# Kernel optimization log

Hardware: AMD Instinct MI355X
Metric: run time of the kernel (lower is better)

Reference implementation:

```python
import jax, jax.numpy as jnp
import numpy as np

N = 50000   # nodes
E = 800000  # edges before self-loops
H = 4       # heads
D = 64      # num_h_feats (per-head out dim of hidden layers)
C = 2       # num_classes
NEG = 0.2   # DGL GATConv leaky_relu negative_slope
EPS = 1e-5  # BatchNorm eps


def setup_inputs() -> dict:
    key = jax.random.key(0)
    ks = jax.random.split(key, 16)
    inp = {}
    inp['feats'] = jax.random.normal(ks[0], (N, 9), jnp.float32)
    inp['W1'] = jax.random.normal(ks[1], (9, H * D), jnp.float32) * 0.1
    inp['al1'] = jax.random.normal(ks[2], (H, D), jnp.float32) * 0.1
    inp['ar1'] = jax.random.normal(ks[3], (H, D), jnp.float32) * 0.1
    inp['b1'] = jnp.zeros((H, D), jnp.float32)
    inp['Wm'] = jax.random.normal(ks[4], (D, H * D), jnp.float32) * 0.1
    inp['alm'] = jax.random.normal(ks[5], (H, D), jnp.float32) * 0.1
    inp['arm'] = jax.random.normal(ks[6], (H, D), jnp.float32) * 0.1
    inp['bm'] = jnp.zeros((H, D), jnp.float32)
    inp['W2'] = jax.random.normal(ks[7], (D, H * C), jnp.float32) * 0.1
    inp['al2'] = jax.random.normal(ks[8], (H, C), jnp.float32) * 0.1
    inp['ar2'] = jax.random.normal(ks[9], (H, C), jnp.float32) * 0.1
    inp['b2'] = jnp.zeros((H, C), jnp.float32)
    inp['gamma'] = jnp.ones((D,), jnp.float32)
    inp['beta'] = jnp.zeros((D,), jnp.float32)
    inp['src'] = jax.random.randint(ks[10], (E,), 0, N, jnp.int32)
    inp['dst'] = jax.random.randint(ks[11], (E,), 0, N, jnp.int32)
    return inp


def gat_layer(x, W, al, ar, b, src, dst, out_d):
    """DGL GATConv: linear -> per-edge attention -> dst-softmax -> scatter-sum."""
    n = x.shape[0]
    z = (x @ W).reshape(n, H, out_d)                 # [N, H, Dout]
    el = jnp.sum(z * al, axis=-1)                    # [N, H] attn on src
    er = jnp.sum(z * ar, axis=-1)                    # [N, H] attn on dst
    e = jax.nn.leaky_relu(el[src] + er[dst], NEG)    # [E, H]
    m = jax.ops.segment_max(e, dst, num_segments=n)  # per-dst max (stable softmax)
    a = jnp.exp(e - m[dst])
    s = jax.ops.segment_sum(a, dst, num_segments=n)
    alpha = a / s[dst]                               # [E, H]
    out = jax.ops.segment_sum(alpha[:, :, None] * z[src], dst, num_segments=n)
    return out + b                                   # [N, H, Dout]


def batchnorm(h, gamma, beta):
    mu = jnp.mean(h, axis=0)
    var = jnp.var(h, axis=0)
    return (h - mu) * jax.lax.rsqrt(var + EPS) * gamma + beta


def reference(feats, W1, al1, ar1, b1, Wm, alm, arm, bm, W2, al2, ar2, b2,
              gamma, beta, src, dst):
    # dgl.add_self_loop
    loop = jnp.arange(N, dtype=src.dtype)
    s = jnp.concatenate([src, loop])
    d = jnp.concatenate([dst, loop])
    h = gat_layer(feats, W1, al1, ar1, b1, s, d, D).sum(axis=1)  # head-sum
    h = batchnorm(h, gamma, beta)
    h = gat_layer(h, Wm, alm, arm, bm, s, d, D).sum(axis=1)
    h = batchnorm(h, gamma, beta)
    o = gat_layer(h, W2, al2, ar2, b2, s, d, C).sum(axis=1)      # [N, C]
    return o
```

## Files before the change

### kernel.cpp

```cpp
#include <hip/hip_runtime.h>
#include <hip/hip_bf16.h>

typedef __hip_bfloat16 bf16;
typedef __bf16 bf16x8 __attribute__((ext_vector_type(8)));
typedef float f32x4 __attribute__((ext_vector_type(4)));
typedef _Float16 h16;
typedef _Float16 h16x4 __attribute__((ext_vector_type(4)));

#define LOG2E 1.44269504088896340736f

__device__ __forceinline__ float b2f(bf16 v) { return __bfloat162float(v); }

__device__ __forceinline__ float ldin(const void* p, size_t i, int isb) {
    return isb ? b2f(((const bf16*)p)[i]) : ((const float*)p)[i];
}
__device__ __forceinline__ unsigned short f2bfbits(float f) {
    bf16 v = __float2bfloat16(f);
    return *(unsigned short*)&v;
}

__global__ __launch_bounds__(256) void fused_prep_lin1_kernel(
    const void* __restrict__ feats, const void* __restrict__ W1,
    const void* __restrict__ Wm,
    const void* __restrict__ al1, const void* __restrict__ ar1,
    const void* __restrict__ alm, const void* __restrict__ arm,
    const unsigned* __restrict__ gbits,
    const int* __restrict__ dstv, int* __restrict__ deg,
    unsigned short* __restrict__ WmT,
    float* __restrict__ alfm, float* __restrict__ arfm,
    h16* __restrict__ zh, float* __restrict__ zc,
    float* __restrict__ el, float* __restrict__ er,
    int* __restrict__ flag, int Nn, int E, int NT) {
    __shared__ h16 zs[16 * 256];
    int isb = (gbits[0] == 0x3F803F80u) ? 1 : 0;
    int tid = threadIdx.x;
    long t = (long)blockIdx.x * 256 + tid;
    if (t == 0) *flag = isb;

    long b1 = (long)E + 2048;
    long b2 = b1 + 256;
    long b3 = b2 + 268;
    if (t < E) {
        atomicAdd(&deg[dstv[t]], 1);
    } else if (t < b1) {
        long u = t - E;
        int col = (int)(u >> 3), k0 = ((int)u & 7) * 8;
        union { unsigned short us[8]; uint4 v; } o;
#pragma unroll
        for (int j = 0; j < 8; j++) {
            int k = k0 + j;
            o.us[j] = f2bfbits(ldin(Wm, (size_t)k * 256 + col, isb));
        }
        *(uint4*)(WmT + u * 8) = o.v;
    } else if (t < b2) {
        int u = (int)(t - b1);
        alfm[u] = ldin(alm, u, isb) * LOG2E;
        arfm[u] = ldin(arm, u, isb) * LOG2E;
    } else if (t < b3) {
        long u = t - b2;
        if (u < 4) {
            el[(size_t)Nn * 4 + u] = -1e30f;
        } else if (u < 260) {
            ((unsigned short*)zh)[(size_t)Nn * 256 + (u - 4)] = 0;
        } else {
            zc[(size_t)Nn * 8 + (u - 260)] = 0.f;
        }
    }

    if (blockIdx.x >= NT) return;
    int w = tid >> 6;
    int l = tid & 63;
    int quad = l >> 4, lc = l & 15;
    int node0 = blockIdx.x * 16;

    int mrow = node0 + lc; if (mrow >= Nn) mrow = Nn - 1;
    union { unsigned short s[8]; bf16x8 v; } ua;
#pragma unroll
    for (int j = 0; j < 8; j++) {
        int k = quad * 8 + j;
        ua.s[j] = (k < 9) ? f2bfbits(ldin(feats, (size_t)mrow * 9 + k, isb))
                          : (unsigned short)0;
    }
    bf16x8 a0 = ua.v;

    float pe[4] = {0.f, 0.f, 0.f, 0.f}, pr[4] = {0.f, 0.f, 0.f, 0.f};
    int row0 = quad * 4;
#pragma unroll
    for (int ct = 0; ct < 4; ++ct) {
        int col = w * 64 + ct * 16 + lc;
        union { unsigned short s[8]; bf16x8 v; } ub;
#pragma unroll
        for (int j = 0; j < 8; j++) {
            int k = quad * 8 + j;
            ub.s[j] = (k < 9) ? f2bfbits(ldin(W1, (size_t)k * 256 + col, isb))
                              : (unsigned short)0;
        }
        f32x4 c = {0.f, 0.f, 0.f, 0.f};
        c = __builtin_amdgcn_mfma_f32_16x16x32_bf16(a0, ub.v, c, 0, 0, 0);
        float av = ldin(al1, col, isb) * LOG2E;
        float rv = ldin(ar1, col, isb) * LOG2E;
#pragma unroll
        for (int r = 0; r < 4; ++r) {
            pe[r] = fmaf(c[r], av, pe[r]);
            pr[r] = fmaf(c[r], rv, pr[r]);
            zs[(row0 + r) * 256 + col] = (h16)c[r];
        }
    }
#pragma unroll
    for (int o = 1; o < 16; o <<= 1) {
#pragma unroll
        for (int r = 0; r < 4; ++r) {
            pe[r] += __shfl_xor(pe[r], o);
            pr[r] += __shfl_xor(pr[r], o);
        }
    }
    if (lc == 0) {
#pragma unroll
        for (int r = 0; r < 4; ++r) {
            int n = node0 + row0 + r;
            if (n < Nn) { el[n * 4 + w] = pe[r]; er[n * 4 + w] = pr[r]; }
        }
    }
    __syncthreads();
#pragma unroll
    for (int it = 0; it < 2; ++it) {
        int flat = it * 2048 + tid * 8;
        int row = flat >> 8;
        if (node0 + row < Nn)
            *(uint4*)(zh + (size_t)node0 * 256 + flat) = *(const uint4*)(zs + flat);
    }
}

__global__ __launch_bounds__(256) void scan1_kernel(
    const int* __restrict__ deg, int* __restrict__ off, int* __restrict__ bsum, int Nn) {
    __shared__ int s[256];
    int t = threadIdx.x, i = blockIdx.x * 256 + t;
    int v = (i < Nn) ? ((deg[i] + 3) & ~3) : 0;
    s[t] = v; __syncthreads();
#pragma unroll
    for (int o = 1; o < 256; o <<= 1) {
        int a = (t >= o) ? s[t - o] : 0;
        __syncthreads();
        s[t] += a;
        __syncthreads();
    }
    if (i < Nn) off[i] = s[t];
    if (t == 255) bsum[blockIdx.x] = s[255];
}

__global__ __launch_bounds__(256) void scan3_kernel(
    const int* __restrict__ deg, int* __restrict__ off, int* __restrict__ cur,
    int* __restrict__ adj, const int* __restrict__ bsum, int Nn, int NB) {
    __shared__ int s[256];
    int t = threadIdx.x;
    int v = (t < NB) ? bsum[t] : 0;
    s[t] = v; __syncthreads();
#pragma unroll
    for (int o = 1; o < 256; o <<= 1) {
        int a = (t >= o) ? s[t - o] : 0;
        __syncthreads();
        s[t] += a;
        __syncthreads();
    }
    s[t] -= v;
    __syncthreads();
    int base = s[blockIdx.x];
    int i = blockIdx.x * 256 + t;
    if (i < Nn) {
        int d = deg[i], pd = (d + 3) & ~3;
        int ex = off[i] - pd + base;
        off[i] = ex;
        cur[i] = ex;
        for (int j = d; j < pd; j++) adj[ex + j] = Nn;
        if (i == Nn - 1) {
            int tot = ex + pd;
            off[Nn] = tot;
            for (int j = 0; j < 32; j++) adj[tot + j] = Nn;
        }
    }
}

__global__ __launch_bounds__(256) void scatter_kernel(
    const int* __restrict__ src, const int* __restrict__ dst,
    int* __restrict__ cur, int* __restrict__ adj, int E) {
    int t = blockIdx.x * 256 + threadIdx.x;
    if (t < E) {
        int p = atomicAdd(&cur[dst[t]], 1);
        adj[p] = src[t];
    }
}

__global__ __launch_bounds__(256) void lin_mfma_bn_kernel(
    const float* __restrict__ x,
    const float* __restrict__ bnsum, const float* __restrict__ bnsumsq,
    const void* __restrict__ gamma, const void* __restrict__ beta,
    const unsigned short* __restrict__ WT,
    const float* __restrict__ alf, const float* __restrict__ arf,
    h16* __restrict__ zh, float* __restrict__ el, float* __restrict__ er,
    const int* __restrict__ flag, int Nn) {
    __shared__ h16 zs[16 * 256];
    __shared__ __align__(16) float scs[64], shs[64];
    int tid = threadIdx.x;
    if (tid < 64) {
        int isb = *flag;
        float inv_n = 1.f / (float)Nn;
        float mu = bnsum[tid] * inv_n;
        float var = bnsumsq[tid] * inv_n - mu * mu;
        float s = rsqrtf(var + 1e-5f) * ldin(gamma, tid, isb);
        scs[tid] = s;
        shs[tid] = ldin(beta, tid, isb) - mu * s;
    }
    __syncthreads();

    int w = tid >> 6;
    int l = tid & 63;
    int quad = l >> 4, lc = l & 15;
    int node0 = blockIdx.x * 16;

    int mrow = node0 + lc; if (mrow >= Nn) mrow = Nn - 1;
    const float* xr = x + (size_t)mrow * 64 + quad * 8;
    float4 f0 = ((const float4*)xr)[0];
    float4 f1 = ((const float4*)xr)[1];
    float4 f2 = ((const float4*)(xr + 32))[0];
    float4 f3 = ((const float4*)(xr + 32))[1];
    float4 s0 = ((const float4*)(scs + quad * 8))[0];
    float4 s1 = ((const float4*)(scs + quad * 8))[1];
    float4 s2 = ((const float4*)(scs + 32 + quad * 8))[0];
    float4 s3 = ((const float4*)(scs + 32 + quad * 8))[1];
    float4 h0 = ((const float4*)(shs + quad * 8))[0];
    float4 h1 = ((const float4*)(shs + quad * 8))[1];
    float4 h2 = ((const float4*)(shs + 32 + quad * 8))[0];
    float4 h3 = ((const float4*)(shs + 32 + quad * 8))[1];

    union { bf16x8 v; unsigned short s[8]; } ua, ub;
    ua.s[0] = f2bfbits(fmaf(f0.x, s0.x, h0.x));
    ua.s[1] = f2bfbits(fmaf(f0.y, s0.y, h0.y));
    ua.s[2] = f2bfbits(fmaf(f0.z, s0.z, h0.z));
    ua.s[3] = f2bfbits(fmaf(f0.w, s0.w, h0.w));
    ua.s[4] = f2bfbits(fmaf(f1.x, s1.x, h1.x));
    ua.s[5] = f2bfbits(fmaf(f1.y, s1.y, h1.y));
    ua.s[6] = f2bfbits(fmaf(f1.z, s1.z, h1.z));
    ua.s[7] = f2bfbits(fmaf(f1.w, s1.w, h1.w));
    ub.s[0] = f2bfbits(fmaf(f2.x, s2.x, h2.x));
    ub.s[1] = f2bfbits(fmaf(f2.y, s2.y, h2.y));
    ub.s[2] = f2bfbits(fmaf(f2.z, s2.z, h2.z));
    ub.s[3] = f2bfbits(fmaf(f2.w, s2.w, h2.w));
    ub.s[4] = f2bfbits(fmaf(f3.x, s3.x, h3.x));
    ub.s[5] = f2bfbits(fmaf(f3.y, s3.y, h3.y));
    ub.s[6] = f2bfbits(fmaf(f3.z, s3.z, h3.z));
    ub.s[7] = f2bfbits(fmaf(f3.w, s3.w, h3.w));
    bf16x8 a0 = ua.v, a1 = ub.v;

    float pe[4] = {0.f, 0.f, 0.f, 0.f}, pr[4] = {0.f, 0.f, 0.f, 0.f};
    int row0 = quad * 4;
#pragma unroll
    for (int ct = 0; ct < 4; ++ct) {
        int col = w * 64 + ct * 16 + lc;
        const bf16x8* wb = (const bf16x8*)(WT + (size_t)col * 64);
        bf16x8 b0 = wb[quad];
        bf16x8 b1 = wb[quad + 4];
        f32x4 c = {0.f, 0.f, 0.f, 0.f};
        c = __builtin_amdgcn_mfma_f32_16x16x32_bf16(a0, b0, c, 0, 0, 0);
        c = __builtin_amdgcn_mfma_f32_16x16x32_bf16(a1, b1, c, 0, 0, 0);
        float av = alf[col], rv = arf[col];
#pragma unroll
        for (int r = 0; r < 4; ++r) {
            pe[r] = fmaf(c[r], av, pe[r]);
            pr[r] = fmaf(c[r], rv, pr[r]);
            zs[(row0 + r) * 256 + col] = (h16)c[r];
        }
    }
#pragma unroll
    for (int o = 1; o < 16; o <<= 1) {
#pragma unroll
        for (int r = 0; r < 4; ++r) {
            pe[r] += __shfl_xor(pe[r], o);
            pr[r] += __shfl_xor(pr[r], o);
        }
    }
    if (lc == 0) {
#pragma unroll
        for (int r = 0; r < 4; ++r) {
            int n = node0 + row0 + r;
            if (n < Nn) { el[n * 4 + w] = pe[r]; er[n * 4 + w] = pr[r]; }
        }
    }
    __syncthreads();
#pragma unroll
    for (int it = 0; it < 2; ++it) {
        int flat = it * 2048 + threadIdx.x * 8;
        int row = flat >> 8;
        if (node0 + row < Nn)
            *(uint4*)(zh + (size_t)node0 * 256 + flat) = *(const uint4*)(zs + flat);
    }
}

__global__ __launch_bounds__(256) void bnstats_kernel(
    const float* __restrict__ x, float* __restrict__ bnsum, float* __restrict__ bnsumsq,
    int Nn) {
    __shared__ float ssum[4][64], ssq[4][64];
    int tid = threadIdx.x;
    int d = tid & 63, r = tid >> 6;
    float s = 0.f, q = 0.f;
    int stride = gridDim.x * 4;
    for (int n = blockIdx.x * 4 + r; n < Nn; n += stride) {
        float v = x[(size_t)n * 64 + d];
        s += v;
        q = fmaf(v, v, q);
    }
    ssum[r][d] = s; ssq[r][d] = q;
    __syncthreads();
    if (tid < 64) {
        float ts = ssum[0][tid] + ssum[1][tid] + ssum[2][tid] + ssum[3][tid];
        float tq = ssq[0][tid] + ssq[1][tid] + ssq[2][tid] + ssq[3][tid];
        atomicAdd(&bnsum[tid], ts);
        atomicAdd(&bnsumsq[tid], tq);
    }
}

__global__ __launch_bounds__(256) void lin3_kernel(
    const float* __restrict__ x,
    const float* __restrict__ bnsum, const float* __restrict__ bnsumsq,
    const void* __restrict__ gamma, const void* __restrict__ beta,
    const void* __restrict__ W, const void* __restrict__ al, const void* __restrict__ ar,
    float* __restrict__ zc, float* __restrict__ el, float* __restrict__ er,
    const int* __restrict__ flag, int Nn) {
    __shared__ __align__(16) float scs[64], shs[64];
    int isb = *flag;
    int tid = threadIdx.x;
    if (tid < 64) {
        float inv_n = 1.f / (float)Nn;
        float mu = bnsum[tid] * inv_n;
        float var = bnsumsq[tid] * inv_n - mu * mu;
        float s = rsqrtf(var + 1e-5f) * ldin(gamma, tid, isb);
        scs[tid] = s;
        shs[tid] = ldin(beta, tid, isb) - mu * s;
    }
    __syncthreads();
    int t = blockIdx.x * 256 + tid;
    if (t >= Nn * 4) return;
    int n = t >> 2, h = t & 3;
    const float4* xr4 = (const float4*)(x + (size_t)n * 64);
    float a0 = 0.f, a1 = 0.f;
#pragma unroll 4
    for (int kk = 0; kk < 16; kk++) {
        float4 xv = xr4[kk];
        int k = kk * 4;
        float xn;
        xn = fmaf(xv.x, scs[k + 0], shs[k + 0]);
        a0 += xn * ldin(W, (k + 0) * 8 + h * 2, isb);
        a1 += xn * ldin(W, (k + 0) * 8 + h * 2 + 1, isb);
        xn = fmaf(xv.y, scs[k + 1], shs[k + 1]);
        a0 += xn * ldin(W, (k + 1) * 8 + h * 2, isb);
        a1 += xn * ldin(W, (k + 1) * 8 + h * 2 + 1, isb);
        xn = fmaf(xv.z, scs[k + 2], shs[k + 2]);
        a0 += xn * ldin(W, (k + 2) * 8 + h * 2, isb);
        a1 += xn * ldin(W, (k + 2) * 8 + h * 2 + 1, isb);
        xn = fmaf(xv.w, scs[k + 3], shs[k + 3]);
        a0 += xn * ldin(W, (k + 3) * 8 + h * 2, isb);
        a1 += xn * ldin(W, (k + 3) * 8 + h * 2 + 1, isb);
    }
    zc[n * 8 + h * 2 + 0] = a0;
    zc[n * 8 + h * 2 + 1] = a1;
    el[t] = (a0 * ldin(al, h * 2, isb) + a1 * ldin(al, h * 2 + 1, isb)) * LOG2E;
    er[t] = (a0 * ldin(ar, h * 2, isb) + a1 * ldin(ar, h * 2 + 1, isb)) * LOG2E;
}

#define GATH(ev, zv, sv)                                        \
    {                                                           \
        ev[0] = el[sv.x * 4 + h]; ev[1] = el[sv.y * 4 + h];     \
        ev[2] = el[sv.z * 4 + h]; ev[3] = el[sv.w * 4 + h];     \
        zv[0] = zrow[(size_t)sv.x * 64 + l];                    \
        zv[1] = zrow[(size_t)sv.y * 64 + l];                    \
        zv[2] = zrow[(size_t)sv.z * 64 + l];                    \
        zv[3] = zrow[(size_t)sv.w * 64 + l];                    \
    }
#define COMP(ev, zv)                                        \
    {                                                       \
        _Pragma("unroll") for (int j = 0; j < 4; j++) {     \
            float e = ev[j] + ern;                          \
            e = fmaxf(e, 0.2f * e);                         \
            float wj = __builtin_amdgcn_exp2f(e);           \
            lsum += wj;                                     \
            acc.x = fmaf(wj, (float)zv[j].x, acc.x);        \
            acc.y = fmaf(wj, (float)zv[j].y, acc.y);        \
            acc.z = fmaf(wj, (float)zv[j].z, acc.z);        \
            acc.w = fmaf(wj, (float)zv[j].w, acc.w);        \
        }                                                   \
    }

__global__ __launch_bounds__(256) void gat_agg64_kernel(
    const h16* __restrict__ zh, const float* __restrict__ el, const float* __restrict__ er,
    const int* __restrict__ off, const int* __restrict__ adj, const void* __restrict__ bias,
    float* __restrict__ x, const int* __restrict__ flag, int Nn, int total_waves) {
    int isb = *flag;
    int tid = threadIdx.x;
    int l = tid & 63;
    int h = l >> 4;
    int gw = blockIdx.x * 4 + (tid >> 6);
    const h16x4* zrow = (const h16x4*)zh;

    float4 bsl;
    bsl.x = ldin(bias, l * 4 + 0, isb);
    bsl.y = ldin(bias, l * 4 + 1, isb);
    bsl.z = ldin(bias, l * 4 + 2, isb);
    bsl.w = ldin(bias, l * 4 + 3, isb);

    if (gw >= Nn) return;

    int n = gw;
    int fs0 = off[n], fs1 = off[n + 1];
    float fel = el[n * 4 + h], fer = er[n * 4 + h];
    int4 fsv = *(const int4*)(adj + fs0);

    while (true) {
        int s0 = fs0;
        int nb = (fs1 - fs0) >> 2;
        float eln = fel, ern = fer;
        int4 svA = fsv;
        h16x4 zself = zrow[(size_t)n * 64 + l];
        int nn = n + total_waves;
        if (nn < Nn) {
            fs0 = off[nn]; fs1 = off[nn + 1];
            fel = el[nn * 4 + h]; fer = er[nn * 4 + h];
            fsv = *(const int4*)(adj + fs0);
        }

        float e0 = eln + ern;
        e0 = fmaxf(e0, 0.2f * e0);
        float w0 = __builtin_amdgcn_exp2f(e0);
        float lsum = w0;
        float4 acc = {0.f, 0.f, 0.f, 0.f};

        if (nb > 0) {
            float evA[4], evB[4];
            h16x4 zvA[4], zvB[4];
            GATH(evA, zvA, svA);
            int4 svB = *(const int4*)(adj + s0 + 4);
            int k = 0;
            while (true) {
                if (k + 1 < nb) GATH(evB, zvB, svB);
                svA = *(const int4*)(adj + s0 + (k + 2) * 4);
                COMP(evA, zvA);
                if (++k >= nb) break;
                if (k + 1 < nb) GATH(evA, zvA, svA);
                svB = *(const int4*)(adj + s0 + (k + 2) * 4);
                COMP(evB, zvB);
                if (++k >= nb) break;
            }
        }

        acc.x = fmaf(w0, (float)zself.x, acc.x);
        acc.y = fmaf(w0, (float)zself.y, acc.y);
        acc.z = fmaf(w0, (float)zself.z, acc.z);
        acc.w = fmaf(w0, (float)zself.w, acc.w);

        float inv = 1.f / lsum;
        float4 r;
        r.x = fmaf(acc.x, inv, bsl.x);
        r.y = fmaf(acc.y, inv, bsl.y);
        r.z = fmaf(acc.z, inv, bsl.z);
        r.w = fmaf(acc.w, inv, bsl.w);
#pragma unroll
        for (int o = 16; o < 64; o <<= 1) {
            r.x += __shfl_xor(r.x, o);
            r.y += __shfl_xor(r.y, o);
            r.z += __shfl_xor(r.z, o);
            r.w += __shfl_xor(r.w, o);
        }
        if (h == 0) ((float4*)(x + (size_t)n * 64))[l & 15] = r;
        if (nn >= Nn) break;
        n = nn;
    }
}
#undef GATH
#undef COMP

#define GATH2(ev, zv, sv)                                       \
    {                                                           \
        ev[0] = el[sv.x * 4 + h]; zv[0] = zc2[sv.x * 4 + h];    \
        ev[1] = el[sv.y * 4 + h]; zv[1] = zc2[sv.y * 4 + h];    \
        ev[2] = el[sv.z * 4 + h]; zv[2] = zc2[sv.z * 4 + h];    \
        ev[3] = el[sv.w * 4 + h]; zv[3] = zc2[sv.w * 4 + h];    \
    }
#define COMP2(ev, zv)                                       \
    {                                                       \
        _Pragma("unroll") for (int j = 0; j < 4; j++) {     \
            float e = ev[j] + er_nh;                        \
            e = fmaxf(e, 0.2f * e);                         \
            float w = __builtin_amdgcn_exp2f(e);            \
            lsum += w;                                      \
            a0 = fmaf(w, zv[j].x, a0);                      \
            a1 = fmaf(w, zv[j].y, a1);                      \
        }                                                   \
    }

__global__ __launch_bounds__(256) void gat_agg2_kernel(
    const float* __restrict__ zc, const float* __restrict__ el, const float* __restrict__ er,
    const int* __restrict__ off, const int* __restrict__ adj, const void* __restrict__ bias,
    void* __restrict__ out, const int* __restrict__ flag, int Nn) {
    int isb = *flag;
    int t = blockIdx.x * 256 + threadIdx.x;
    if (t >= Nn * 4) return;
    int n = t >> 2, h = t & 3;
    const float2* zc2 = (const float2*)zc;
    float er_nh = er[n * 4 + h];
    float e0 = el[n * 4 + h] + er_nh;
    e0 = fmaxf(e0, 0.2f * e0);
    float w0 = __builtin_amdgcn_exp2f(e0);
    float lsum = w0;
    float2 zn = zc2[n * 4 + h];
    float a0 = w0 * zn.x, a1 = w0 * zn.y;
    int s0 = off[n];
    int nb = (off[n + 1] - s0) >> 2;
    if (nb > 0) {
        float evA[4], evB[4], evC[4];
        float2 zvA[4], zvB[4], zvC[4];
        int4 svA = *(const int4*)(adj + s0);
        GATH2(evA, zvA, svA);
        int4 svB = *(const int4*)(adj + s0 + 4);
        if (nb > 1) GATH2(evB, zvB, svB);
        int4 svC = *(const int4*)(adj + s0 + 8);
        int k = 0;
        while (true) {
            if (k + 2 < nb) GATH2(evC, zvC, svC);
            svA = *(const int4*)(adj + s0 + (k + 3) * 4);
            COMP2(evA, zvA);
            if (++k >= nb) break;
            if (k + 2 < nb) GATH2(evA, zvA, svA);
            svB = *(const int4*)(adj + s0 + (k + 3) * 4);
            COMP2(evB, zvB);
            if (++k >= nb) break;
            if (k + 2 < nb) GATH2(evB, zvB, svB);
            svC = *(const int4*)(adj + s0 + (k + 3) * 4);
            COMP2(evC, zvC);
            if (++k >= nb) break;
        }
    }
    float inv = 1.f / lsum;
    float v0 = fmaf(a0, inv, ldin(bias, h * 2 + 0, isb));
    float v1 = fmaf(a1, inv, ldin(bias, h * 2 + 1, isb));
#pragma unroll
    for (int o = 1; o < 4; o <<= 1) {
        v0 += __shfl_xor(v0, o);
        v1 += __shfl_xor(v1, o);
    }
    if (h == 0) {
        if (isb) {
            ((bf16*)out)[n * 2 + 0] = __float2bfloat16(v0);
            ((bf16*)out)[n * 2 + 1] = __float2bfloat16(v1);
        } else {
            ((float*)out)[n * 2 + 0] = v0;
            ((float*)out)[n * 2 + 1] = v1;
        }
    }
}
#undef GATH2
#undef COMP2

extern "C" void kernel_launch(void* const* d_in, const int* in_sizes, int n_in,
                              void* d_out, int out_size, void* d_ws, size_t ws_size,
                              hipStream_t stream) {
    const void* feats = d_in[0];
    const void* W1    = d_in[1];
    const void* al1   = d_in[2];
    const void* ar1   = d_in[3];
    const void* b1    = d_in[4];
    const void* Wm    = d_in[5];
    const void* alm   = d_in[6];
    const void* arm   = d_in[7];
    const void* bm    = d_in[8];
    const void* W2    = d_in[9];
    const void* al2   = d_in[10];
    const void* ar2   = d_in[11];
    const void* b2v   = d_in[12];
    const void* gamma = d_in[13];
    const void* beta  = d_in[14];
    const int*  src   = (const int*)d_in[15];
    const int*  dst   = (const int*)d_in[16];

    int Nn = in_sizes[0] / 9;
    int E  = in_sizes[15];

    float* ws = (float*)d_ws;
    h16*   zh   = (h16*)ws;
    float* zc   = ws + (size_t)(Nn + 1) * 128;
    float* el   = zc + (size_t)Nn * 8 + 8;
    float* er   = el + (size_t)Nn * 4 + 4;
    float* x    = er + (size_t)Nn * 4;
    int*   deg  = (int*)(x + (size_t)Nn * 64);
    float* bns1 = (float*)(deg + Nn);
    float* bnq1 = bns1 + 64;
    float* bns2 = bnq1 + 64;
    float* bnq2 = bns2 + 64;
    size_t msetBytes = (size_t)Nn * 4 + 256 * 4;
    float* alfm = bnq2 + 64;
    float* arfm = alfm + 256;
    unsigned short* WmT =
        (unsigned short*)(((uintptr_t)(arfm + 256) + 15) & ~(uintptr_t)15);
    int*   flag = (int*)(WmT + 256 * 64);
    int*   off  = flag + 1;
    int*   cur  = off + Nn + 1;
    int*   adj  = (int*)(((uintptr_t)(cur + Nn) + 15) & ~(uintptr_t)15);
    int*   bsum = adj + E + 3 * Nn + 32;

    dim3 B(256);
    int NB1 = (Nn + 255) / 256;
    int gE  = (E + 255) / 256;
    int gMF = (Nn + 15) / 16;
    int gN4 = (Nn * 4 + 255) / 256;
    long fusedN = (long)E + 2048 + 256 + 268;
    int gFused = (int)((fusedN + 255) / 256);
    int AGG_GRID = 2048;
    int total_waves = AGG_GRID * 4;

    hipMemsetAsync(deg, 0, msetBytes, stream);

    fused_prep_lin1_kernel<<<gFused, B, 0, stream>>>(
        feats, W1, Wm, al1, ar1, alm, arm, (const unsigned*)gamma,
        dst, deg, WmT, alfm, arfm, zh, zc, el, er, flag, Nn, E, gMF);

    scan1_kernel<<<NB1, B, 0, stream>>>(deg, off, bsum, Nn);
    scan3_kernel<<<NB1, B, 0, stream>>>(deg, off, cur, adj, bsum, Nn, NB1);
    scatter_kernel<<<gE, B, 0, stream>>>(src, dst, cur, adj, E);

    gat_agg64_kernel<<<AGG_GRID, B, 0, stream>>>(
        zh, el, er, off, adj, b1, x, flag, Nn, total_waves);
    bnstats_kernel<<<512, B, 0, stream>>>(x, bns1, bnq1, Nn);

    lin_mfma_bn_kernel<<<gMF, B, 0, stream>>>(x, bns1, bnq1, gamma, beta,
                                              WmT, alfm, arfm, zh, el, er, flag, Nn);
    gat_agg64_kernel<<<AGG_GRID, B, 0, stream>>>(
        zh, el, er, off, adj, bm, x, flag, Nn, total_waves);
    bnstats_kernel<<<512, B, 0, stream>>>(x, bns2, bnq2, Nn);

    lin3_kernel<<<gN4, B, 0, stream>>>(x, bns2, bnq2, gamma, beta,
                                       W2, al2, ar2, zc, el, er, flag, Nn);
    gat_agg2_kernel<<<gN4, B, 0, stream>>>(zc, el, er, off, adj, b2v, d_out, flag, Nn);
}
```

Measured before the change: 441.3 us.

## Fuse CSR scan and scatter into one kernel with grid-wide barriers

```diff
diff --git a/kernel.cpp b/kernel.cpp
--- a/kernel.cpp
+++ b/kernel.cpp
@@ -131,12 +131,20 @@
     }
 }
 
-__global__ __launch_bounds__(256) void scan1_kernel(
-    const int* __restrict__ deg, int* __restrict__ off, int* __restrict__ bsum, int Nn) {
+__global__ __launch_bounds__(256) void csr_build_kernel(
+    const int* __restrict__ deg, const int* __restrict__ src,
+    const int* __restrict__ dst,
+    int* __restrict__ off, int* __restrict__ cur, int* __restrict__ adj,
+    int* __restrict__ bsum, int* __restrict__ ctr,
+    int Nn, int E, int NB) {
     __shared__ int s[256];
-    int t = threadIdx.x, i = blockIdx.x * 256 + t;
-    int v = (i < Nn) ? ((deg[i] + 3) & ~3) : 0;
-    s[t] = v; __syncthreads();
+    int t = threadIdx.x;
+    int bid = blockIdx.x;
+    int i = bid * 256 + t;
+    int d = (i < Nn) ? deg[i] : 0;
+    int pd = (d + 3) & ~3;
+
+    s[t] = pd; __syncthreads();
 #pragma unroll
     for (int o = 1; o < 256; o <<= 1) {
         int a = (t >= o) ? s[t - o] : 0;
@@ -144,16 +152,21 @@
         s[t] += a;
         __syncthreads();
     }
-    if (i < Nn) off[i] = s[t];
-    if (t == 255) bsum[blockIdx.x] = s[255];
-}
-
-__global__ __launch_bounds__(256) void scan3_kernel(
-    const int* __restrict__ deg, int* __restrict__ off, int* __restrict__ cur,
-    int* __restrict__ adj, const int* __restrict__ bsum, int Nn, int NB) {
-    __shared__ int s[256];
-    int t = threadIdx.x;
-    int v = (t < NB) ? bsum[t] : 0;
+    int incl = s[t];
+    if (t == 255) {
+        bsum[bid] = s[255];
+        __threadfence();
+        __hip_atomic_fetch_add(&ctr[0], 1, __ATOMIC_RELEASE, __HIP_MEMORY_SCOPE_AGENT);
+    }
+    if (t == 0) {
+        while (__hip_atomic_load(&ctr[0], __ATOMIC_ACQUIRE, __HIP_MEMORY_SCOPE_AGENT) < NB)
+            __builtin_amdgcn_s_sleep(2);
+    }
+    __syncthreads();
+
+    int v = (t < NB) ? __hip_atomic_load(&bsum[t], __ATOMIC_RELAXED,
+                                         __HIP_MEMORY_SCOPE_AGENT)
+                     : 0;
     s[t] = v; __syncthreads();
 #pragma unroll
     for (int o = 1; o < 256; o <<= 1) {
@@ -164,11 +177,9 @@
     }
     s[t] -= v;
     __syncthreads();
-    int base = s[blockIdx.x];
-    int i = blockIdx.x * 256 + t;
+    int base = s[bid];
     if (i < Nn) {
-        int d = deg[i], pd = (d + 3) & ~3;
-        int ex = off[i] - pd + base;
+        int ex = incl - pd + base;
         off[i] = ex;
         cur[i] = ex;
         for (int j = d; j < pd; j++) adj[ex + j] = Nn;
@@ -178,15 +189,31 @@
             for (int j = 0; j < 32; j++) adj[tot + j] = Nn;
         }
     }
-}
-
-__global__ __launch_bounds__(256) void scatter_kernel(
-    const int* __restrict__ src, const int* __restrict__ dst,
-    int* __restrict__ cur, int* __restrict__ adj, int E) {
-    int t = blockIdx.x * 256 + threadIdx.x;
-    if (t < E) {
-        int p = atomicAdd(&cur[dst[t]], 1);
-        adj[p] = src[t];
+    __threadfence();
+    __syncthreads();
+    if (t == 0) {
+        __hip_atomic_fetch_add(&ctr[1], 1, __ATOMIC_RELEASE, __HIP_MEMORY_SCOPE_AGENT);
+        while (__hip_atomic_load(&ctr[1], __ATOMIC_ACQUIRE, __HIP_MEMORY_SCOPE_AGENT) < NB)
+            __builtin_amdgcn_s_sleep(2);
+    }
+    __syncthreads();
+
+    long stride = (long)NB * 256;
+    long e = (long)bid * 256 + t;
+    for (; e + 3 * stride < E; e += 4 * stride) {
+        int d0 = dst[e];              int s0v = src[e];
+        int d1 = dst[e + stride];     int s1v = src[e + stride];
+        int d2 = dst[e + 2 * stride]; int s2v = src[e + 2 * stride];
+        int d3 = dst[e + 3 * stride]; int s3v = src[e + 3 * stride];
+        int p0 = atomicAdd(&cur[d0], 1);
+        int p1 = atomicAdd(&cur[d1], 1);
+        int p2 = atomicAdd(&cur[d2], 1);
+        int p3 = atomicAdd(&cur[d3], 1);
+        adj[p0] = s0v; adj[p1] = s1v; adj[p2] = s2v; adj[p3] = s3v;
+    }
+    for (; e < E; e += stride) {
+        int p = atomicAdd(&cur[dst[e]], 1);
+        adj[p] = src[e];
     }
 }
 
@@ -593,8 +620,9 @@
     float* bnq1 = bns1 + 64;
     float* bns2 = bnq1 + 64;
     float* bnq2 = bns2 + 64;
-    size_t msetBytes = (size_t)Nn * 4 + 256 * 4;
-    float* alfm = bnq2 + 64;
+    int*   ctr  = (int*)(bnq2 + 64);
+    size_t msetBytes = (size_t)Nn * 4 + 256 * 4 + 8;
+    float* alfm = (float*)(ctr + 2);
     float* arfm = alfm + 256;
     unsigned short* WmT =
         (unsigned short*)(((uintptr_t)(arfm + 256) + 15) & ~(uintptr_t)15);
@@ -606,7 +634,6 @@
 
     dim3 B(256);
     int NB1 = (Nn + 255) / 256;
-    int gE  = (E + 255) / 256;
     int gMF = (Nn + 15) / 16;
     int gN4 = (Nn * 4 + 255) / 256;
     long fusedN = (long)E + 2048 + 256 + 268;
@@ -620,9 +647,8 @@
         feats, W1, Wm, al1, ar1, alm, arm, (const unsigned*)gamma,
         dst, deg, WmT, alfm, arfm, zh, zc, el, er, flag, Nn, E, gMF);
 
-    scan1_kernel<<<NB1, B, 0, stream>>>(deg, off, bsum, Nn);
-    scan3_kernel<<<NB1, B, 0, stream>>>(deg, off, cur, adj, bsum, Nn, NB1);
-    scatter_kernel<<<gE, B, 0, stream>>>(src, dst, cur, adj, E);
+    csr_build_kernel<<<NB1, B, 0, stream>>>(deg, src, dst, off, cur, adj,
+                                            bsum, ctr, Nn, E, NB1);
 
     gat_agg64_kernel<<<AGG_GRID, B, 0, stream>>>(
         zh, el, er, off, adj, b1, x, flag, Nn, total_waves);
```

Result: slower. 483.0 us (+9.5%).
